# Kernel tuning notes

Hardware: AMD Instinct MI355X
Metric: run time of the kernel (lower is better)

## Reference

```python
import jax, jax.numpy as jnp
import numpy as np

D = 768
H = 12
HD = D // H
MLP = 3072
SCALE = 1.0 / np.sqrt(HD)
EPS = 1e-6


def setup_inputs() -> dict:
    key = jax.random.key(0)
    ks = jax.random.split(key, 16)
    s = 0.02
    inp = {
        "x": jax.random.normal(ks[0], (16, 1024, D), dtype=jnp.float32),
        "wq": jax.random.normal(ks[1], (D, D), dtype=jnp.float32) * s,
        "bq": jnp.zeros((D,), jnp.float32),
        "wk": jax.random.normal(ks[2], (D, D), dtype=jnp.float32) * s,
        "bk": jnp.zeros((D,), jnp.float32),
        "wv": jax.random.normal(ks[3], (D, D), dtype=jnp.float32) * s,
        "bv": jnp.zeros((D,), jnp.float32),
        "wo": jax.random.normal(ks[4], (D, D), dtype=jnp.float32) * s,
        "bo": jnp.zeros((D,), jnp.float32),
        "w1": jax.random.normal(ks[5], (D, MLP), dtype=jnp.float32) * s,
        "b1": jax.random.normal(ks[6], (MLP,), dtype=jnp.float32) * 1e-6,
        "w2": jax.random.normal(ks[7], (MLP, D), dtype=jnp.float32) * s,
        "b2": jax.random.normal(ks[8], (D,), dtype=jnp.float32) * 1e-6,
        "ln1_g": jnp.ones((D,), jnp.float32),
        "ln1_b": jnp.zeros((D,), jnp.float32),
        "ln2_g": jnp.ones((D,), jnp.float32),
        "ln2_b": jnp.zeros((D,), jnp.float32),
    }
    return inp


def layer_norm(x, g, b):
    mu = jnp.mean(x, axis=-1, keepdims=True)
    var = jnp.mean(jnp.square(x - mu), axis=-1, keepdims=True)
    return (x - mu) * jax.lax.rsqrt(var + EPS) * g + b


def block_fwd(x, wq, bq, wk, bk, wv, bv, wo, bo, w1, b1, w2, b2,
              ln1_g, ln1_b, ln2_g, ln2_b):
    B, N, _ = x.shape
    res = x
    h = layer_norm(x, ln1_g, ln1_b)
    # QKV projections, split into heads: [B, H, N, HD]
    q = (h @ wq + bq).reshape(B, N, H, HD).transpose(0, 2, 1, 3)
    k = (h @ wk + bk).reshape(B, N, H, HD).transpose(0, 2, 1, 3)
    v = (h @ wv + bv).reshape(B, N, H, HD).transpose(0, 2, 1, 3)
    scores = jnp.einsum("bhqd,bhkd->bhqk", q, k) * SCALE
    probs = jax.nn.softmax(scores, axis=-1)
    ctx = jnp.einsum("bhqk,bhkd->bhqd", probs, v)
    ctx = ctx.transpose(0, 2, 1, 3).reshape(B, N, D)
    attn_out = ctx @ wo + bo
    x = attn_out + res
    res = x
    h = layer_norm(x, ln2_g, ln2_b)
    h = jax.nn.gelu(h @ w1 + b1, approximate=False)
    h = h @ w2 + b2
    return h + res


def reference(x, wq, bq, wk, bk, wv, bv, wo, bo, w1, b1, w2, b2,
              ln1_g, ln1_b, ln2_g, ln2_b):
    return block_fwd(x, wq, bq, wk, bk, wv, bv, wo, bo, w1, b1, w2, b2,
                     ln1_g, ln1_b, ln2_g, ln2_b)
```

## Files before the change

### kernel.cpp

```cpp
#include <hip/hip_runtime.h>
#include <math.h>


#define BS   16
#define SEQ  1024
#define DIM  768
#define NH   12
#define HDM  64
#define MLPD 3072
#define NTOK (BS * SEQ)

typedef unsigned short u16;
typedef __attribute__((ext_vector_type(8))) short bf16x8;
typedef __attribute__((ext_vector_type(4))) float f32x4;

__device__ __forceinline__ float gelu_exact(float x) {
  return 0.5f * x * (1.0f + erff(x * 0.70710678118654752440f));
}
__device__ __forceinline__ u16 f2bf(float f) {
  unsigned u = __float_as_uint(f);
  return (u16)((u + 0x7fffu + ((u >> 16) & 1u)) >> 16);
}
__device__ __forceinline__ float bf2f(u16 h) {
  return __uint_as_float((unsigned)h << 16);
}

__global__ __launch_bounds__(256) void wtrans_kernel(
    const float* __restrict__ W, u16* __restrict__ Wt, int K, int N) {
  __shared__ u16 t[64][65];
  const int k0 = blockIdx.y << 6, n0 = blockIdx.x << 6;
  const int r  = threadIdx.x >> 2;
  const int c4 = (threadIdx.x & 3) << 4;
#pragma unroll
  for (int c = 0; c < 16; c += 4) {
    const float4 v = *(const float4*)(W + (size_t)(k0 + r) * N + n0 + c4 + c);
    t[r][c4 + c + 0] = f2bf(v.x);
    t[r][c4 + c + 1] = f2bf(v.y);
    t[r][c4 + c + 2] = f2bf(v.z);
    t[r][c4 + c + 3] = f2bf(v.w);
  }
  __syncthreads();
  unsigned wbuf[8];
#pragma unroll
  for (int p = 0; p < 8; ++p)
    wbuf[p] = (unsigned)t[c4 + 2 * p][r] | ((unsigned)t[c4 + 2 * p + 1][r] << 16);
  uint4* dst = (uint4*)(Wt + (size_t)(n0 + r) * K + k0 + c4);
  dst[0] = make_uint4(wbuf[0], wbuf[1], wbuf[2], wbuf[3]);
  dst[1] = make_uint4(wbuf[4], wbuf[5], wbuf[6], wbuf[7]);
}

__global__ __launch_bounds__(256) void ln_kernel(
    const float* __restrict__ x, const float* __restrict__ g,
    const float* __restrict__ b, u16* __restrict__ out) {
  const int lane = threadIdx.x & 63;
  const int wv   = threadIdx.x >> 6;
  const int tok  = (blockIdx.x << 2) + wv;
  const float4* xr = (const float4*)(x + (size_t)tok * DIM);
  float4 a0 = xr[lane], a1 = xr[lane + 64], a2 = xr[lane + 128];
  float s  = a0.x + a0.y + a0.z + a0.w + a1.x + a1.y + a1.z + a1.w
           + a2.x + a2.y + a2.z + a2.w;
  float s2 = a0.x*a0.x + a0.y*a0.y + a0.z*a0.z + a0.w*a0.w
           + a1.x*a1.x + a1.y*a1.y + a1.z*a1.z + a1.w*a1.w
           + a2.x*a2.x + a2.y*a2.y + a2.z*a2.z + a2.w*a2.w;
#pragma unroll
  for (int o = 32; o; o >>= 1) {
    s  += __shfl_xor(s,  o, 64);
    s2 += __shfl_xor(s2, o, 64);
  }
  const float mu   = s * (1.0f / DIM);
  const float rstd = rsqrtf(s2 * (1.0f / DIM) - mu * mu + 1e-6f);
  const float4* gp = (const float4*)g;
  const float4* bp = (const float4*)b;
  ushort4* op = (ushort4*)(out + (size_t)tok * DIM);
#define LN_EMIT(av, idx)                                                       \
  {                                                                            \
    const float4 gv = gp[idx]; const float4 bv = bp[idx]; ushort4 ov;          \
    ov.x = f2bf((av.x - mu) * rstd * gv.x + bv.x);                             \
    ov.y = f2bf((av.y - mu) * rstd * gv.y + bv.y);                             \
    ov.z = f2bf((av.z - mu) * rstd * gv.z + bv.z);                             \
    ov.w = f2bf((av.w - mu) * rstd * gv.w + bv.w);                             \
    op[idx] = ov;                                                              \
  }
  LN_EMIT(a0, lane);
  LN_EMIT(a1, lane + 64);
  LN_EMIT(a2, lane + 128);
#undef LN_EMIT
}

__device__ __forceinline__ void stage128x32(const u16* gtile, int ldk,
                                            u16* lds, int tid) {
#pragma unroll
  for (int i = 0; i < 2; ++i) {
    const int b = i * 4096 + tid * 16;
    const int row = b >> 6;
    const int chunk = (b >> 4) & 3;
    const u16* src = gtile + (size_t)row * ldk + chunk * 8;
    u16* dst = lds + ((i * 4096 + (tid >> 6) * 1024) >> 1);
    __builtin_amdgcn_global_load_lds((const void*)src, (void*)dst, 16, 0, 0);
  }
}

template <int EPI, int OUTBF>
__global__ __launch_bounds__(256) void mm_kernel(
    const u16* __restrict__ A, const u16* __restrict__ Wt,
    const float* __restrict__ bias, const float* res, void* outp,
    int M, int K, int Nc) {
  __shared__ __align__(16) u16 As[2][128 * 32];
  __shared__ __align__(16) u16 Bs[2][128 * 32];
  const int tid  = threadIdx.x;
  const int lane = tid & 63;
  const int wid  = tid >> 6;
  const int wr   = (wid >> 1) << 6;
  const int wc   = (wid & 1) << 6;
  const int row0 = blockIdx.y << 7;
  const int col0 = blockIdx.x << 7;
  const int fr   = lane & 15;
  const int kch  = lane >> 4;
  const u16* Ab = A  + (size_t)row0 * K;
  const u16* Bb = Wt + (size_t)col0 * K;
  const int nkt = K >> 5;

  f32x4 acc[4][4];
#pragma unroll
  for (int i = 0; i < 4; ++i)
#pragma unroll
    for (int j = 0; j < 4; ++j) acc[i][j] = {0.f, 0.f, 0.f, 0.f};

  stage128x32(Ab, K, As[0], tid);
  stage128x32(Bb, K, Bs[0], tid);
  __syncthreads();

  int cur = 0;
  for (int kt = 0; kt < nkt; ++kt) {
    if (kt + 1 < nkt) {
      stage128x32(Ab + (kt + 1) * 32, K, As[cur ^ 1], tid);
      stage128x32(Bb + (kt + 1) * 32, K, Bs[cur ^ 1], tid);
    }
    bf16x8 af[4], bf[4];
#pragma unroll
    for (int f = 0; f < 4; ++f) {
      af[f] = *(const bf16x8*)&As[cur][(wr + (f << 4) + fr) * 32 + (kch << 3)];
      bf[f] = *(const bf16x8*)&Bs[cur][(wc + (f << 4) + fr) * 32 + (kch << 3)];
    }
#pragma unroll
    for (int i = 0; i < 4; ++i)
#pragma unroll
      for (int j = 0; j < 4; ++j)
        acc[i][j] = __builtin_amdgcn_mfma_f32_16x16x32_bf16(af[i], bf[j],
                                                            acc[i][j], 0, 0, 0);
    __syncthreads();
    cur ^= 1;
  }

  float* outf = (float*)outp;
  u16*   outb = (u16*)outp;
#pragma unroll
  for (int jf = 0; jf < 4; ++jf) {
    const int c = col0 + wc + (jf << 4) + fr;
    const float bv = bias[c];
#pragma unroll
    for (int i = 0; i < 4; ++i) {
#pragma unroll
      for (int j = 0; j < 4; ++j) {
        const int r = row0 + wr + (i << 4) + ((lane >> 4) << 2) + j;
        float v = acc[i][jf][j] + bv;
        if (EPI == 1) v += res[(size_t)r * Nc + c];
        if (EPI == 2) v = gelu_exact(v);
        if (OUTBF) outb[(size_t)r * Nc + c] = f2bf(v);
        else       outf[(size_t)r * Nc + c] = v;
      }
    }
  }
}

__device__ __forceinline__ int swz(int row, int chunk) {
  return row * 128 + ((chunk ^ (row & 7)) << 4);
}

__global__ __launch_bounds__(256) void attn_kernel(
    const u16* __restrict__ q, const u16* __restrict__ k,
    const u16* __restrict__ v, u16* __restrict__ ctx) {
  __shared__ __align__(16) u16 Qs[4096];
  __shared__ __align__(16) u16 Ks[4096];
  __shared__ __align__(16) u16 Vt[4096];
  __shared__ __align__(16) u16 Ps[4096];
  const int tid  = threadIdx.x;
  const int lane = tid & 63;
  const int w    = tid >> 6;
  const int fr   = lane & 15;
  const int g    = lane >> 4;
  const int qt = blockIdx.x, h = blockIdx.y, b = blockIdx.z;
  const size_t hbase = (size_t)b * SEQ * DIM + (size_t)h * HDM;
  const int srow = tid >> 2;
  const int sc   = (tid & 3) << 4;
  const int sch  = sc >> 3;

  {
    const u16* qp = q + hbase + (size_t)(qt * 64 + srow) * DIM + sc;
    const uint4 q0 = *(const uint4*)qp;
    const uint4 q1 = *(const uint4*)(qp + 8);
    *(uint4*)((char*)Qs + swz(srow, sch))     = q0;
    *(uint4*)((char*)Qs + swz(srow, sch + 1)) = q1;
  }

  float m_[4] = {-INFINITY, -INFINITY, -INFINITY, -INFINITY};
  float l_[4] = {0.f, 0.f, 0.f, 0.f};
  f32x4 oacc[4];
#pragma unroll
  for (int f = 0; f < 4; ++f) oacc[f] = {0.f, 0.f, 0.f, 0.f};

  for (int kt = 0; kt < SEQ / 64; ++kt) {
    __syncthreads();
    {
      const u16* kp = k + hbase + (size_t)(kt * 64 + srow) * DIM + sc;
      const uint4 k0 = *(const uint4*)kp;
      const uint4 k1 = *(const uint4*)(kp + 8);
      *(uint4*)((char*)Ks + swz(srow, sch))     = k0;
      *(uint4*)((char*)Ks + swz(srow, sch + 1)) = k1;
      const u16* vp = v + hbase + (size_t)(kt * 64 + srow) * DIM + sc;
      const uint4 v0 = *(const uint4*)vp;
      const uint4 v1 = *(const uint4*)(vp + 8);
      const unsigned uw[8] = {v0.x, v0.y, v0.z, v0.w, v1.x, v1.y, v1.z, v1.w};
#pragma unroll
      for (int e = 0; e < 16; ++e) {
        const u16 val = (e & 1) ? (u16)(uw[e >> 1] >> 16)
                                : (u16)(uw[e >> 1] & 0xffffu);
        const int d = sc + e;
        *(u16*)((char*)Vt + ((d * 128 + srow * 2) ^ ((d & 7) << 4))) = val;
      }
    }
    __syncthreads();

    f32x4 sacc[4];
#pragma unroll
    for (int f = 0; f < 4; ++f) sacc[f] = {0.f, 0.f, 0.f, 0.f};
    bf16x8 aq[2];
#pragma unroll
    for (int s = 0; s < 2; ++s)
      aq[s] = *(const bf16x8*)((char*)Qs + swz(w * 16 + fr, s * 4 + g));
#pragma unroll
    for (int f = 0; f < 4; ++f)
#pragma unroll
      for (int s = 0; s < 2; ++s) {
        const bf16x8 bk =
            *(const bf16x8*)((char*)Ks + swz(f * 16 + fr, s * 4 + g));
        sacc[f] = __builtin_amdgcn_mfma_f32_16x16x32_bf16(aq[s], bk, sacc[f],
                                                          0, 0, 0);
      }

    float corr[4];
#pragma unroll
    for (int r = 0; r < 4; ++r) {
#pragma unroll
      for (int f = 0; f < 4; ++f) sacc[f][r] *= 0.125f;
      float rm = fmaxf(fmaxf(sacc[0][r], sacc[1][r]),
                       fmaxf(sacc[2][r], sacc[3][r]));
#pragma unroll
      for (int o = 8; o; o >>= 1) rm = fmaxf(rm, __shfl_xor(rm, o, 64));
      const float mnew = fmaxf(m_[r], rm);
      corr[r] = expf(m_[r] - mnew);
      float ps = 0.f;
#pragma unroll
      for (int f = 0; f < 4; ++f) {
        const float p = expf(sacc[f][r] - mnew);
        sacc[f][r] = p;
        ps += p;
      }
#pragma unroll
      for (int o = 8; o; o >>= 1) ps += __shfl_xor(ps, o, 64);
      l_[r] = l_[r] * corr[r] + ps;
      m_[r] = mnew;
#pragma unroll
      for (int f = 0; f < 4; ++f) oacc[f][r] *= corr[r];
    }

#pragma unroll
    for (int f = 0; f < 4; ++f)
#pragma unroll
      for (int r = 0; r < 4; ++r) {
        const int row = w * 16 + g * 4 + r;
        const int col = f * 16 + fr;
        *(u16*)((char*)Ps + ((row * 128 + col * 2) ^ ((row & 7) << 4))) =
            f2bf(sacc[f][r]);
      }

    bf16x8 ap[2];
#pragma unroll
    for (int s = 0; s < 2; ++s)
      ap[s] = *(const bf16x8*)((char*)Ps + swz(w * 16 + fr, s * 4 + g));
#pragma unroll
    for (int f = 0; f < 4; ++f)
#pragma unroll
      for (int s = 0; s < 2; ++s) {
        const bf16x8 bv =
            *(const bf16x8*)((char*)Vt + swz(f * 16 + fr, s * 4 + g));
        oacc[f] = __builtin_amdgcn_mfma_f32_16x16x32_bf16(ap[s], bv, oacc[f],
                                                          0, 0, 0);
      }
  }

  float inv[4];
#pragma unroll
  for (int r = 0; r < 4; ++r) inv[r] = 1.0f / l_[r];
#pragma unroll
  for (int f = 0; f < 4; ++f)
#pragma unroll
    for (int r = 0; r < 4; ++r) {
      const int qrow = qt * 64 + w * 16 + g * 4 + r;
      ctx[hbase + (size_t)qrow * DIM + f * 16 + fr] = f2bf(oacc[f][r] * inv[r]);
    }
}

extern "C" void kernel_launch(void* const* d_in, const int* in_sizes, int n_in,
                              void* d_out, int out_size, void* d_ws,
                              size_t ws_size, hipStream_t stream) {
  const float* x    = (const float*)d_in[0];
  const float* wq   = (const float*)d_in[1];
  const float* bq   = (const float*)d_in[2];
  const float* wk   = (const float*)d_in[3];
  const float* bk   = (const float*)d_in[4];
  const float* wv   = (const float*)d_in[5];
  const float* bv   = (const float*)d_in[6];
  const float* wo   = (const float*)d_in[7];
  const float* bo   = (const float*)d_in[8];
  const float* w1   = (const float*)d_in[9];
  const float* b1   = (const float*)d_in[10];
  const float* w2   = (const float*)d_in[11];
  const float* b2   = (const float*)d_in[12];
  const float* ln1g = (const float*)d_in[13];
  const float* ln1b = (const float*)d_in[14];
  const float* ln2g = (const float*)d_in[15];
  const float* ln2b = (const float*)d_in[16];
  float* out = (float*)d_out;

  const size_t TD = (size_t)NTOK * DIM;
  const size_t S768 = (size_t)DIM * DIM;
  const size_t SMLP = (size_t)DIM * MLPD;
  u16* wtq  = (u16*)d_ws;
  u16* wtk  = wtq + S768;
  u16* wtv  = wtk + S768;
  u16* wto  = wtv + S768;
  u16* wt1  = wto + S768;
  u16* wt2  = wt1 + SMLP;
  u16* tokb = wt2 + SMLP;
  u16* qb   = tokb + TD;
  u16* kb   = qb + TD;
  u16* vb   = kb + TD;

  const dim3 blk(256);
  wtrans_kernel<<<dim3(DIM / 64, DIM / 64), blk, 0, stream>>>(wq, wtq, DIM, DIM);
  wtrans_kernel<<<dim3(DIM / 64, DIM / 64), blk, 0, stream>>>(wk, wtk, DIM, DIM);
  wtrans_kernel<<<dim3(DIM / 64, DIM / 64), blk, 0, stream>>>(wv, wtv, DIM, DIM);
  wtrans_kernel<<<dim3(DIM / 64, DIM / 64), blk, 0, stream>>>(wo, wto, DIM, DIM);
  wtrans_kernel<<<dim3(MLPD / 64, DIM / 64), blk, 0, stream>>>(w1, wt1, DIM, MLPD);
  wtrans_kernel<<<dim3(DIM / 64, MLPD / 64), blk, 0, stream>>>(w2, wt2, MLPD, DIM);
  ln_kernel<<<dim3(NTOK / 4), blk, 0, stream>>>(x, ln1g, ln1b, tokb);
  const dim3 g768(DIM / 128, NTOK / 128);
  mm_kernel<0, 1><<<g768, blk, 0, stream>>>(tokb, wtq, bq, nullptr, qb, NTOK, DIM, DIM);
  mm_kernel<0, 1><<<g768, blk, 0, stream>>>(tokb, wtk, bk, nullptr, kb, NTOK, DIM, DIM);
  mm_kernel<0, 1><<<g768, blk, 0, stream>>>(tokb, wtv, bv, nullptr, vb, NTOK, DIM, DIM);
  attn_kernel<<<dim3(SEQ / 64, NH, BS), blk, 0, stream>>>(qb, kb, vb, tokb);
  mm_kernel<1, 0><<<g768, blk, 0, stream>>>(tokb, wto, bo, x, out, NTOK, DIM, DIM);
  ln_kernel<<<dim3(NTOK / 4), blk, 0, stream>>>(out, ln2g, ln2b, tokb);
  mm_kernel<2, 1><<<dim3(MLPD / 128, NTOK / 128), blk, 0, stream>>>(
      tokb, wt1, b1, nullptr, qb, NTOK, DIM, MLPD);
  mm_kernel<1, 0><<<g768, blk, 0, stream>>>(qb, wt2, b2, out, out, NTOK, MLPD, DIM);
}
```

Before: 862.5 us.

## Emit V pre-transposed from projection GEMM, fold softmax scale into Q, use fast exp

The V projection GEMM gains an epilogue that writes V in a per-head transposed [B,H,HD,N] layout, so the attention kernel stages V into shared memory with two vector stores instead of sixteen scalar transposing stores. The 1/sqrt(d) scale moves into the Q projection epilogue, and softmax switches from expf to __expf. Float-to-bf16 conversion in GEMM epilogues now uses the HIP intrinsic. The MLP intermediate buffer is relocated to a 'big' region that holds Q/K/Vt and is large enough for the 4x-wide MLP output. The transposed V stores are 8-byte writes strided across heads, which may reduce write coalescing in the V GEMM.

```diff
diff --git a/kernel.cpp b/kernel.cpp
--- a/kernel.cpp
+++ b/kernel.cpp
@@ -1,4 +1,5 @@
 #include <hip/hip_runtime.h>
+#include <hip/hip_bf16.h>
 #include <math.h>
 
 
@@ -18,11 +19,14 @@
   return 0.5f * x * (1.0f + erff(x * 0.70710678118654752440f));
 }
 __device__ __forceinline__ u16 f2bf(float f) {
+  __hip_bfloat16 h = __float2bfloat16(f);
+  u16 r;
+  __builtin_memcpy(&r, &h, 2);
+  return r;
+}
+__device__ __forceinline__ u16 f2bf_sw(float f) {
   unsigned u = __float_as_uint(f);
   return (u16)((u + 0x7fffu + ((u >> 16) & 1u)) >> 16);
-}
-__device__ __forceinline__ float bf2f(u16 h) {
-  return __uint_as_float((unsigned)h << 16);
 }
 
 __global__ __launch_bounds__(256) void wtrans_kernel(
@@ -34,10 +38,10 @@
 #pragma unroll
   for (int c = 0; c < 16; c += 4) {
     const float4 v = *(const float4*)(W + (size_t)(k0 + r) * N + n0 + c4 + c);
-    t[r][c4 + c + 0] = f2bf(v.x);
-    t[r][c4 + c + 1] = f2bf(v.y);
-    t[r][c4 + c + 2] = f2bf(v.z);
-    t[r][c4 + c + 3] = f2bf(v.w);
+    t[r][c4 + c + 0] = f2bf_sw(v.x);
+    t[r][c4 + c + 1] = f2bf_sw(v.y);
+    t[r][c4 + c + 2] = f2bf_sw(v.z);
+    t[r][c4 + c + 3] = f2bf_sw(v.w);
   }
   __syncthreads();
   unsigned wbuf[8];
@@ -100,7 +104,7 @@
   }
 }
 
-template <int EPI, int OUTBF>
+template <int EPI>
 __global__ __launch_bounds__(256) void mm_kernel(
     const u16* __restrict__ A, const u16* __restrict__ Wt,
     const float* __restrict__ bias, const float* res, void* outp,
@@ -158,16 +162,32 @@
   for (int jf = 0; jf < 4; ++jf) {
     const int c = col0 + wc + (jf << 4) + fr;
     const float bv = bias[c];
-#pragma unroll
-    for (int i = 0; i < 4; ++i) {
-#pragma unroll
-      for (int j = 0; j < 4; ++j) {
-        const int r = row0 + wr + (i << 4) + ((lane >> 4) << 2) + j;
-        float v = acc[i][jf][j] + bv;
-        if (EPI == 1) v += res[(size_t)r * Nc + c];
-        if (EPI == 2) v = gelu_exact(v);
-        if (OUTBF) outb[(size_t)r * Nc + c] = f2bf(v);
-        else       outf[(size_t)r * Nc + c] = v;
+    if (EPI == 4) {
+      const int hh = c >> 6, dd = c & 63;
+#pragma unroll
+      for (int i = 0; i < 4; ++i) {
+        const int rbase = row0 + wr + (i << 4) + ((lane >> 4) << 2);
+        const int bb = rbase >> 10, n0 = rbase & 1023;
+        ushort4 o;
+        o.x = f2bf(acc[i][jf][0] + bv);
+        o.y = f2bf(acc[i][jf][1] + bv);
+        o.z = f2bf(acc[i][jf][2] + bv);
+        o.w = f2bf(acc[i][jf][3] + bv);
+        *(ushort4*)(outb + ((((size_t)bb * NH + hh) * HDM + dd) << 10) + n0) = o;
+      }
+    } else {
+#pragma unroll
+      for (int i = 0; i < 4; ++i) {
+#pragma unroll
+        for (int j = 0; j < 4; ++j) {
+          const int r = row0 + wr + (i << 4) + ((lane >> 4) << 2) + j;
+          float v = acc[i][jf][j] + bv;
+          if (EPI == 1) v += res[(size_t)r * Nc + c];
+          if (EPI == 2) v = gelu_exact(v);
+          if (EPI == 3) v *= 0.125f;
+          if (EPI == 1) outf[(size_t)r * Nc + c] = v;
+          else          outb[(size_t)r * Nc + c] = f2bf(v);
+        }
       }
     }
   }
@@ -179,7 +199,7 @@
 
 __global__ __launch_bounds__(256) void attn_kernel(
     const u16* __restrict__ q, const u16* __restrict__ k,
-    const u16* __restrict__ v, u16* __restrict__ ctx) {
+    const u16* __restrict__ vt, u16* __restrict__ ctx) {
   __shared__ __align__(16) u16 Qs[4096];
   __shared__ __align__(16) u16 Ks[4096];
   __shared__ __align__(16) u16 Vt[4096];
@@ -191,6 +211,7 @@
   const int g    = lane >> 4;
   const int qt = blockIdx.x, h = blockIdx.y, b = blockIdx.z;
   const size_t hbase = (size_t)b * SEQ * DIM + (size_t)h * HDM;
+  const u16* vhd = vt + ((size_t)(b * NH + h) * HDM) * SEQ;
   const int srow = tid >> 2;
   const int sc   = (tid & 3) << 4;
   const int sch  = sc >> 3;
@@ -217,17 +238,11 @@
       const uint4 k1 = *(const uint4*)(kp + 8);
       *(uint4*)((char*)Ks + swz(srow, sch))     = k0;
       *(uint4*)((char*)Ks + swz(srow, sch + 1)) = k1;
-      const u16* vp = v + hbase + (size_t)(kt * 64 + srow) * DIM + sc;
+      const u16* vp = vhd + (size_t)srow * SEQ + kt * 64 + sc;
       const uint4 v0 = *(const uint4*)vp;
       const uint4 v1 = *(const uint4*)(vp + 8);
-      const unsigned uw[8] = {v0.x, v0.y, v0.z, v0.w, v1.x, v1.y, v1.z, v1.w};
-#pragma unroll
-      for (int e = 0; e < 16; ++e) {
-        const u16 val = (e & 1) ? (u16)(uw[e >> 1] >> 16)
-                                : (u16)(uw[e >> 1] & 0xffffu);
-        const int d = sc + e;
-        *(u16*)((char*)Vt + ((d * 128 + srow * 2) ^ ((d & 7) << 4))) = val;
-      }
+      *(uint4*)((char*)Vt + swz(srow, sch))     = v0;
+      *(uint4*)((char*)Vt + swz(srow, sch + 1)) = v1;
     }
     __syncthreads();
 
@@ -251,18 +266,16 @@
     float corr[4];
 #pragma unroll
     for (int r = 0; r < 4; ++r) {
-#pragma unroll
-      for (int f = 0; f < 4; ++f) sacc[f][r] *= 0.125f;
       float rm = fmaxf(fmaxf(sacc[0][r], sacc[1][r]),
                        fmaxf(sacc[2][r], sacc[3][r]));
 #pragma unroll
       for (int o = 8; o; o >>= 1) rm = fmaxf(rm, __shfl_xor(rm, o, 64));
       const float mnew = fmaxf(m_[r], rm);
-      corr[r] = expf(m_[r] - mnew);
+      corr[r] = __expf(m_[r] - mnew);
       float ps = 0.f;
 #pragma unroll
       for (int f = 0; f < 4; ++f) {
-        const float p = expf(sacc[f][r] - mnew);
+        const float p = __expf(sacc[f][r] - mnew);
         sacc[f][r] = p;
         ps += p;
       }
@@ -343,9 +356,10 @@
   u16* wt1  = wto + S768;
   u16* wt2  = wt1 + SMLP;
   u16* tokb = wt2 + SMLP;
-  u16* qb   = tokb + TD;
-  u16* kb   = qb + TD;
-  u16* vb   = kb + TD;
+  u16* big  = tokb + TD;
+  u16* qb   = big;
+  u16* kb   = big + TD;
+  u16* vtb  = big + 2 * TD;
 
   const dim3 blk(256);
   wtrans_kernel<<<dim3(DIM / 64, DIM / 64), blk, 0, stream>>>(wq, wtq, DIM, DIM);
@@ -356,13 +370,13 @@
   wtrans_kernel<<<dim3(DIM / 64, MLPD / 64), blk, 0, stream>>>(w2, wt2, MLPD, DIM);
   ln_kernel<<<dim3(NTOK / 4), blk, 0, stream>>>(x, ln1g, ln1b, tokb);
   const dim3 g768(DIM / 128, NTOK / 128);
-  mm_kernel<0, 1><<<g768, blk, 0, stream>>>(tokb, wtq, bq, nullptr, qb, NTOK, DIM, DIM);
-  mm_kernel<0, 1><<<g768, blk, 0, stream>>>(tokb, wtk, bk, nullptr, kb, NTOK, DIM, DIM);
-  mm_kernel<0, 1><<<g768, blk, 0, stream>>>(tokb, wtv, bv, nullptr, vb, NTOK, DIM, DIM);
-  attn_kernel<<<dim3(SEQ / 64, NH, BS), blk, 0, stream>>>(qb, kb, vb, tokb);
-  mm_kernel<1, 0><<<g768, blk, 0, stream>>>(tokb, wto, bo, x, out, NTOK, DIM, DIM);
+  mm_kernel<3><<<g768, blk, 0, stream>>>(tokb, wtq, bq, nullptr, qb, NTOK, DIM, DIM);
+  mm_kernel<0><<<g768, blk, 0, stream>>>(tokb, wtk, bk, nullptr, kb, NTOK, DIM, DIM);
+  mm_kernel<4><<<g768, blk, 0, stream>>>(tokb, wtv, bv, nullptr, vtb, NTOK, DIM, DIM);
+  attn_kernel<<<dim3(SEQ / 64, NH, BS), blk, 0, stream>>>(qb, kb, vtb, tokb);
+  mm_kernel<1><<<g768, blk, 0, stream>>>(tokb, wto, bo, x, out, NTOK, DIM, DIM);
   ln_kernel<<<dim3(NTOK / 4), blk, 0, stream>>>(out, ln2g, ln2b, tokb);
-  mm_kernel<2, 1><<<dim3(MLPD / 128, NTOK / 128), blk, 0, stream>>>(
-      tokb, wt1, b1, nullptr, qb, NTOK, DIM, MLPD);
-  mm_kernel<1, 0><<<g768, blk, 0, stream>>>(qb, wt2, b2, out, out, NTOK, MLPD, DIM);
-}
+  mm_kernel<2><<<dim3(MLPD / 128, NTOK / 128), blk, 0, stream>>>(
+      tokb, wt1, b1, nullptr, big, NTOK, DIM, MLPD);
+  mm_kernel<1><<<g768, blk, 0, stream>>>(big, wt2, b2, out, out, NTOK, MLPD, DIM);
+}
```

After: 796.7 us. 7.6% less time.
